# Performance work log

Measured on AMD Instinct MI355X. Metric: run time of the kernel, lower is better.

The kernel has to match this reference:

```python
import jax, jax.numpy as jnp
import numpy as np

B, S, H, E, V = 64, 512, 1024, 512, 32000
D = 2  # bidirectional encoder -> memory dim = D*H


def setup_inputs() -> dict:
    key = jax.random.key(0)
    ks = jax.random.split(key, 16)
    sc = lambda n: 1.0 / np.sqrt(n)
    return {
        "word": jax.random.randint(ks[0], (B,), 1, V),
        "hidden": jax.random.normal(ks[1], (B, H), jnp.float32),
        "encoder_outputs": jax.random.normal(ks[2], (B, S, D * H), jnp.float32),
        "output_distribution": jax.random.uniform(ks[3], (B, V), jnp.float32),
        "encoder_attention": jax.random.uniform(ks[4], (B, S), jnp.float32),
        # embedding (padding_idx=0 row zeroed)
        "emb": jax.random.normal(ks[5], (V, E), jnp.float32).at[0].set(0.0) * 0.02,
        # Bah_Attn params
        "lin1_w": jax.random.normal(ks[6], (H, H), jnp.float32) * sc(H),
        "lin1_b": jnp.zeros((H,), jnp.float32),
        "lin2_w": jax.random.normal(ks[7], (H, D * H), jnp.float32) * sc(D * H),
        "lin2_b": jnp.zeros((H,), jnp.float32),
        "v_w": jax.random.normal(ks[8], (1, H), jnp.float32) * sc(H),
        "v_b": jnp.zeros((1,), jnp.float32),
        # GRUCell params: input = context(2H) + word_vec(E) = 2560
        "W_ih": jax.random.normal(ks[9], (3 * H, D * H + E), jnp.float32) * sc(H),
        "b_ih": jnp.zeros((3 * H,), jnp.float32),
        "W_hh": jax.random.normal(ks[10], (3 * H, H), jnp.float32) * sc(H),
        "b_hh": jnp.zeros((3 * H,), jnp.float32),
        # output projection
        "out_w": jax.random.normal(ks[11], (V, H), jnp.float32) * sc(H),
        "out_b": jnp.zeros((V,), jnp.float32),
    }


def reference(word, hidden, encoder_outputs, output_distribution, encoder_attention,
              emb, lin1_w, lin1_b, lin2_w, lin2_b, v_w, v_b,
              W_ih, b_ih, W_hh, b_hh, out_w, out_b):
    # word embedding lookup (feed_word_emb='word')
    word_vec = emb[word]                                   # [B, E]
    h_x = hidden @ lin1_w.T + lin1_b                       # [B, H]
    h_m = jnp.einsum('bsm,hm->bsh', encoder_outputs, lin2_w) + lin2_b  # [B, S, H]
    e = jnp.tanh(h_x[:, None, :] + h_m) @ v_w[0] + v_b[0]  # [B, S]
    score = jax.nn.softmax(e, axis=-1)                     # [B, S]
    context = jnp.einsum('bs,bsm->bm', score, encoder_outputs)  # [B, 2H]
    # GRUCell step on cat([context, word_vec])
    x = jnp.concatenate([context, word_vec], axis=1)       # [B, 2H+E]
    gi = x @ W_ih.T + b_ih                                 # [B, 3H]
    gh = hidden @ W_hh.T + b_hh                            # [B, 3H]
    i_r, i_z, i_n = jnp.split(gi, 3, axis=1)
    h_r, h_z, h_n = jnp.split(gh, 3, axis=1)
    r = jax.nn.sigmoid(i_r + h_r)
    z = jax.nn.sigmoid(i_z + h_z)
    n = jnp.tanh(i_n + r * h_n)
    new_hidden = (1.0 - z) * n + z * hidden                # [B, H]
    pred_word = new_hidden @ out_w.T + out_b               # [B, V]
    return (pred_word, new_hidden, score)
```

## Files before the change

### kernel.cpp

```cpp
#include <hip/hip_runtime.h>
#include <hip/hip_bf16.h>
#include <stdint.h>

typedef __attribute__((ext_vector_type(4))) float f32x4;
typedef __attribute__((ext_vector_type(8))) short short8;

#define B_   64
#define S_   512
#define H_   1024
#define E_   512
#define V_   32000
#define M_   2048
#define BS_  32768
#define XIN_ 2560
#define G3_  3072

__device__ __forceinline__ unsigned short f2bf(float f) {
  union { float f; unsigned u; } x; x.f = f;
  unsigned r = x.u + 0x7fffu + ((x.u >> 16) & 1u);
  return (unsigned short)(r >> 16);
}

__device__ __forceinline__ float bf2f(unsigned short u) {
  union { unsigned u; float f; } x; x.u = (unsigned)u << 16; return x.f;
}

__device__ __forceinline__ void async16(const void* g, void* l) {
  __builtin_amdgcn_global_load_lds((const __attribute__((address_space(1))) unsigned*)g,
                                   (__attribute__((address_space(3))) unsigned*)l,
                                   16, 0, 0);
}

__global__ __launch_bounds__(256) void k_conv(const float* __restrict__ enc,
                                              unsigned short* __restrict__ ebf,
                                              const float* __restrict__ lin2w,
                                              unsigned short* __restrict__ bw,
                                              const int* __restrict__ word,
                                              const float* __restrict__ emb,
                                              float* __restrict__ wv) {
  const size_t NENC8 = (size_t)BS_ * M_ / 8;
  const size_t NW8   = (size_t)H_ * M_ / 8;
  const size_t NWV4  = (size_t)B_ * E_ / 4;
  const size_t total = NENC8 + NW8 + NWV4;
  for (size_t idx = (size_t)blockIdx.x * 256 + threadIdx.x; idx < total;
       idx += (size_t)gridDim.x * 256) {
    if (idx < NENC8) {
      f32x4 a = *(const f32x4*)(enc + idx * 8);
      f32x4 b = *(const f32x4*)(enc + idx * 8 + 4);
      short8 o = { (short)f2bf(a.x), (short)f2bf(a.y), (short)f2bf(a.z), (short)f2bf(a.w),
                   (short)f2bf(b.x), (short)f2bf(b.y), (short)f2bf(b.z), (short)f2bf(b.w) };
      *(short8*)(ebf + idx * 8) = o;
    } else if (idx < NENC8 + NW8) {
      size_t i = idx - NENC8;
      f32x4 a = *(const f32x4*)(lin2w + i * 8);
      f32x4 b = *(const f32x4*)(lin2w + i * 8 + 4);
      short8 o = { (short)f2bf(a.x), (short)f2bf(a.y), (short)f2bf(a.z), (short)f2bf(a.w),
                   (short)f2bf(b.x), (short)f2bf(b.y), (short)f2bf(b.z), (short)f2bf(b.w) };
      *(short8*)(bw + i * 8) = o;
    } else {
      size_t i = idx - NENC8 - NW8;
      int i0 = (int)i * 4;
      int b = i0 >> 9, c = i0 & 511;
      f32x4 v = *(const f32x4*)(emb + (size_t)word[b] * E_ + c);
      *(f32x4*)(wv + i0) = v;
    }
  }
}

__global__ __launch_bounds__(256) void k_hx(const float* __restrict__ hidden,
                                            const float* __restrict__ w1,
                                            const float* __restrict__ b1,
                                            const float* __restrict__ b2,
                                            float* __restrict__ hx) {
  __shared__ float hs[64][36];
  __shared__ float Ws[64][36];
  const int t = threadIdx.x;
  const int hbase = blockIdx.x * 64;
  const int hb = t & 15, bb = t >> 4;
  const int srow = t >> 2, sc0 = (t & 3) * 8;
  float acc[4][4] = {};
  for (int kc = 0; kc < H_; kc += 32) {
    *(f32x4*)&hs[srow][sc0]     = *(const f32x4*)(hidden + (size_t)srow * H_ + kc + sc0);
    *(f32x4*)&hs[srow][sc0 + 4] = *(const f32x4*)(hidden + (size_t)srow * H_ + kc + sc0 + 4);
    *(f32x4*)&Ws[srow][sc0]     = *(const f32x4*)(w1 + (size_t)(hbase + srow) * H_ + kc + sc0);
    *(f32x4*)&Ws[srow][sc0 + 4] = *(const f32x4*)(w1 + (size_t)(hbase + srow) * H_ + kc + sc0 + 4);
    __syncthreads();
#pragma unroll
    for (int kk = 0; kk < 32; ++kk) {
      float a[4], w4[4];
#pragma unroll
      for (int i = 0; i < 4; ++i) a[i] = hs[bb * 4 + i][kk];
#pragma unroll
      for (int j = 0; j < 4; ++j) w4[j] = Ws[hb + 16 * j][kk];
#pragma unroll
      for (int i = 0; i < 4; ++i)
#pragma unroll
        for (int j = 0; j < 4; ++j) acc[i][j] += a[i] * w4[j];
    }
    __syncthreads();
  }
#pragma unroll
  for (int i = 0; i < 4; ++i)
#pragma unroll
    for (int j = 0; j < 4; ++j) {
      int h = hbase + hb + 16 * j;
      hx[(size_t)(bb * 4 + i) * H_ + h] = acc[i][j] + b1[h] + b2[h];
    }
}

__global__ __launch_bounds__(256) void k_attn_bf(const unsigned short* __restrict__ encbf,
                                                 const unsigned short* __restrict__ bw,
                                                 const float* __restrict__ hx,
                                                 const float* __restrict__ vw,
                                                 float* __restrict__ epart) {
  __shared__ unsigned short As[3][4096];
  __shared__ unsigned short Bs[3][4096];
  const int bid = blockIdx.x;
  const int xcd = bid & 7, idx = bid >> 3;
  const int bm = xcd * 32 + (idx >> 3);
  const int bn = idx & 7;
  const int t = threadIdx.x;
  const int l = t & 63, w = t >> 6;
  const int wr = w >> 1, wc = w & 1;
  const int l15 = l & 15, l4 = l >> 4;

  f32x4 acc[4][4] = {};

  const unsigned short* Ag = encbf + (size_t)(bm * 128) * M_;
  const unsigned short* Bg = bw + (size_t)(bn * 128) * M_;

  const int srow = t >> 2;
  const int sc = ((t & 3) ^ ((t >> 3) & 3)) * 8;
  const unsigned short* ApT = Ag + (size_t)srow * M_ + sc;
  const unsigned short* BpT = Bg + (size_t)srow * M_ + sc;
  const int xoff = (l4 ^ ((l15 >> 1) & 3)) * 8;

#define STAGE(buf, kt) do { const int k0 = (kt) * 32;                    \
    async16(ApT + k0,             &As[buf][0]    + (size_t)t * 8);       \
    async16(ApT + 64 * M_ + k0,   &As[buf][2048] + (size_t)t * 8);       \
    async16(BpT + k0,             &Bs[buf][0]    + (size_t)t * 8);       \
    async16(BpT + 64 * M_ + k0,   &Bs[buf][2048] + (size_t)t * 8); } while (0)

  STAGE(0, 0);
  STAGE(1, 1);
  asm volatile("s_waitcnt vmcnt(4)" ::: "memory");
  __builtin_amdgcn_s_barrier();

  int cur = 0;
  for (int kt = 0; kt < 64; ++kt) {
    int nx2 = cur + 2; if (nx2 >= 3) nx2 -= 3;
    if (kt < 62) STAGE(nx2, kt + 2);
    short8 af[4], bf[4];
#pragma unroll
    for (int m = 0; m < 4; ++m)
      af[m] = *(const short8*)(&As[cur][(wr * 64 + m * 16 + l15) * 32 + xoff]);
#pragma unroll
    for (int n = 0; n < 4; ++n)
      bf[n] = *(const short8*)(&Bs[cur][(wc * 64 + n * 16 + l15) * 32 + xoff]);
#pragma unroll
    for (int m = 0; m < 4; ++m)
#pragma unroll
      for (int n = 0; n < 4; ++n)
        acc[m][n] = __builtin_amdgcn_mfma_f32_16x16x32_bf16(af[m], bf[n], acc[m][n], 0, 0, 0);
    if (kt < 62) {
      asm volatile("s_waitcnt vmcnt(4)" ::: "memory");
    } else {
      asm volatile("s_waitcnt vmcnt(0)" ::: "memory");
    }
    __builtin_amdgcn_s_barrier();
    cur = cur + 1; if (cur >= 3) cur = 0;
  }
#undef STAGE

  const int colbase = bn * 128 + wc * 64;
#pragma unroll
  for (int m = 0; m < 4; ++m) {
#pragma unroll
    for (int j = 0; j < 4; ++j) {
      int rloc = wr * 64 + m * 16 + l4 * 4 + j;
      int rg = bm * 128 + rloc;
      int b = rg >> 9;
      float sum = 0.f;
#pragma unroll
      for (int n = 0; n < 4; ++n) {
        int h = colbase + n * 16 + l15;
        sum += vw[h] * tanhf(hx[b * H_ + h] + acc[m][n][j]);
      }
      sum += __shfl_xor(sum, 1);
      sum += __shfl_xor(sum, 2);
      sum += __shfl_xor(sum, 4);
      sum += __shfl_xor(sum, 8);
      if (l15 == 0) epart[(size_t)(bn * 2 + wc) * BS_ + rg] = sum;
    }
  }
}

__global__ __launch_bounds__(256) void k_attn(const float* __restrict__ enc,
                                              const unsigned short* __restrict__ bw,
                                              const float* __restrict__ hx,
                                              const float* __restrict__ vw,
                                              float* __restrict__ epart) {
  __shared__ unsigned short As[128 * 32];
  __shared__ unsigned short Bs[128 * 32];
  const int bid = blockIdx.x;
  const int bm = bid & 255, bn = bid >> 8;
  const int t = threadIdx.x;
  const int l = t & 63, w = t >> 6;
  const int wr = w >> 1, wc = w & 1;
  const int l15 = l & 15, l4 = l >> 4;

  f32x4 acc[4][4] = {};

  const float* Ag = enc + (size_t)(bm * 128) * M_;
  const unsigned short* Bg = bw + (size_t)(bn * 128) * M_;

  const int ar = t >> 3;
  const int ac = (t & 7) * 4;
  const int br = t >> 2;
  const int bc = (t & 3) * 8;

  for (int kt = 0; kt < 64; ++kt) {
    const int k0 = kt * 32;
    async16(Bg + (size_t)br * M_ + k0 + bc, (char*)Bs + (size_t)t * 16);
    async16(Bg + (size_t)(br + 64) * M_ + k0 + bc, (char*)Bs + 4096 + (size_t)t * 16);
#pragma unroll
    for (int j = 0; j < 4; ++j) {
      f32x4 v = *(const f32x4*)(Ag + (size_t)(ar + j * 32) * M_ + k0 + ac);
      ushort4 o = { f2bf(v.x), f2bf(v.y), f2bf(v.z), f2bf(v.w) };
      *(ushort4*)(As + (ar + j * 32) * 32 + ac) = o;
    }
    __syncthreads();
    short8 af[4], bf[4];
#pragma unroll
    for (int m = 0; m < 4; ++m)
      af[m] = *(const short8*)(As + (wr * 64 + m * 16 + l15) * 32 + l4 * 8);
#pragma unroll
    for (int n = 0; n < 4; ++n)
      bf[n] = *(const short8*)(Bs + (wc * 64 + n * 16 + l15) * 32 + l4 * 8);
#pragma unroll
    for (int m = 0; m < 4; ++m)
#pragma unroll
      for (int n = 0; n < 4; ++n)
        acc[m][n] = __builtin_amdgcn_mfma_f32_16x16x32_bf16(af[m], bf[n], acc[m][n], 0, 0, 0);
    __syncthreads();
  }

  const int colbase = bn * 128 + wc * 64;
#pragma unroll
  for (int m = 0; m < 4; ++m) {
#pragma unroll
    for (int j = 0; j < 4; ++j) {
      int rloc = wr * 64 + m * 16 + l4 * 4 + j;
      int rg = bm * 128 + rloc;
      int b = rg >> 9;
      float sum = 0.f;
#pragma unroll
      for (int n = 0; n < 4; ++n) {
        int h = colbase + n * 16 + l15;
        sum += vw[h] * tanhf(hx[b * H_ + h] + acc[m][n][j]);
      }
      sum += __shfl_xor(sum, 1);
      sum += __shfl_xor(sum, 2);
      sum += __shfl_xor(sum, 4);
      sum += __shfl_xor(sum, 8);
      if (l15 == 0) epart[(size_t)(bn * 2 + wc) * BS_ + rg] = sum;
    }
  }
}

__global__ __launch_bounds__(256) void k_softmax(const float* __restrict__ epart,
                                                 float* __restrict__ score) {
  int b = blockIdx.x, t = threadIdx.x;
  float v0 = 0.f, v1 = 0.f;
#pragma unroll
  for (int p = 0; p < 16; ++p) {
    v0 += epart[(size_t)p * BS_ + b * S_ + t];
    v1 += epart[(size_t)p * BS_ + b * S_ + 256 + t];
  }
  int w = t >> 6, l = t & 63;
  float m = fmaxf(v0, v1);
#pragma unroll
  for (int off = 32; off; off >>= 1) m = fmaxf(m, __shfl_xor(m, off));
  __shared__ float sm[4];
  __shared__ float ssum[4];
  if (l == 0) sm[w] = m;
  __syncthreads();
  float M = fmaxf(fmaxf(sm[0], sm[1]), fmaxf(sm[2], sm[3]));
  float p0 = expf(v0 - M), p1 = expf(v1 - M);
  float s = p0 + p1;
#pragma unroll
  for (int off = 32; off; off >>= 1) s += __shfl_xor(s, off);
  if (l == 0) ssum[w] = s;
  __syncthreads();
  float inv = 1.f / (ssum[0] + ssum[1] + ssum[2] + ssum[3]);
  score[b * S_ + t] = p0 * inv;
  score[b * S_ + 256 + t] = p1 * inv;
}

__global__ __launch_bounds__(256) void k_ctxb(const unsigned short* __restrict__ encbf,
                                              const float* __restrict__ score,
                                              float* __restrict__ cpart) {
  int blk = blockIdx.x;
  int b = blk >> 3, sc = blk & 7;
  int t = threadIdx.x;
  int m = t * 8;
  f32x4 acc0 = {0.f, 0.f, 0.f, 0.f}, acc1 = {0.f, 0.f, 0.f, 0.f};
  const unsigned short* ep = encbf + (size_t)(b * S_ + sc * 64) * M_ + m;
  const float* sp = score + b * S_ + sc * 64;
#pragma unroll 4
  for (int s8 = 0; s8 < 64; ++s8) {
    float sv = sp[s8];
    short8 v = *(const short8*)(ep + (size_t)s8 * M_);
    acc0.x += bf2f((unsigned short)v[0]) * sv;
    acc0.y += bf2f((unsigned short)v[1]) * sv;
    acc0.z += bf2f((unsigned short)v[2]) * sv;
    acc0.w += bf2f((unsigned short)v[3]) * sv;
    acc1.x += bf2f((unsigned short)v[4]) * sv;
    acc1.y += bf2f((unsigned short)v[5]) * sv;
    acc1.z += bf2f((unsigned short)v[6]) * sv;
    acc1.w += bf2f((unsigned short)v[7]) * sv;
  }
  float* dst = cpart + (size_t)sc * (B_ * M_) + b * M_ + m;
  *(f32x4*)dst = acc0;
  *(f32x4*)(dst + 4) = acc1;
}

__global__ __launch_bounds__(256) void k_ctx(const float* __restrict__ enc,
                                             const float* __restrict__ score,
                                             float* __restrict__ cpart) {
  int blk = blockIdx.x;
  int b = blk >> 4, mc = (blk >> 3) & 1, sc = blk & 7;
  int t = threadIdx.x;
  int m = mc * 1024 + t * 4;
  f32x4 acc = {0.f, 0.f, 0.f, 0.f};
  const float* ep = enc + (size_t)b * S_ * M_ + m;
  const float* sp = score + b * S_ + sc * 64;
#pragma unroll 4
  for (int s8 = 0; s8 < 64; ++s8) {
    float sv = sp[s8];
    f32x4 v = *(const f32x4*)(ep + (size_t)(sc * 64 + s8) * M_);
    acc += v * sv;
  }
  *(f32x4*)(cpart + (size_t)sc * (B_ * M_) + b * M_ + m) = acc;
}

__global__ void k_ctxred(const float* __restrict__ cpart, float* __restrict__ ctx) {
  int i0 = (blockIdx.x * 256 + threadIdx.x) * 4;
  f32x4 a = {0.f, 0.f, 0.f, 0.f};
#pragma unroll
  for (int p = 0; p < 8; ++p) a += *(const f32x4*)(cpart + (size_t)p * (B_ * M_) + i0);
  *(f32x4*)(ctx + i0) = a;
}

__global__ __launch_bounds__(256) void k_grugemm(const float* __restrict__ ctx,
                                                 const float* __restrict__ wv,
                                                 const float* __restrict__ hidden,
                                                 const float* __restrict__ Wih,
                                                 const float* __restrict__ bih,
                                                 const float* __restrict__ Whh,
                                                 const float* __restrict__ bhh,
                                                 float* __restrict__ gi0,
                                                 float* __restrict__ gi1,
                                                 float* __restrict__ gh0,
                                                 float* __restrict__ gh1) {
  __shared__ float xs[64][36];
  __shared__ float Ws[64][36];
  const int t = threadIdx.x;
  const int blk = blockIdx.x;
  const bool ghh = blk >= 96;
  const int sub = ghh ? blk - 96 : blk;
  const int colt = sub % 48, half = sub / 48;
  const int gbase = colt * 64;
  const int K = ghh ? H_ : XIN_;
  const int klo = ghh ? (half ? 512 : 0) : (half ? 1280 : 0);
  const int khi = ghh ? (half ? 1024 : 512) : (half ? 2560 : 1280);
  const float* Wp = ghh ? Whh : Wih;
  const int vb = t & 15, bb = t >> 4;
  const int srow = t >> 2, sc0 = (t & 3) * 8;
  float acc[4][4] = {};
  for (int kc = klo; kc < khi; kc += 32) {
    f32x4 xa, xb;
    if (ghh) {
      xa = *(const f32x4*)(hidden + (size_t)srow * H_ + kc + sc0);
      xb = *(const f32x4*)(hidden + (size_t)srow * H_ + kc + sc0 + 4);
    } else if (kc + sc0 < M_) {
      xa = *(const f32x4*)(ctx + (size_t)srow * M_ + kc + sc0);
      xb = *(const f32x4*)(ctx + (size_t)srow * M_ + kc + sc0 + 4);
    } else {
      xa = *(const f32x4*)(wv + (size_t)srow * E_ + kc + sc0 - M_);
      xb = *(const f32x4*)(wv + (size_t)srow * E_ + kc + sc0 - M_ + 4);
    }
    *(f32x4*)&xs[srow][sc0] = xa;
    *(f32x4*)&xs[srow][sc0 + 4] = xb;
    *(f32x4*)&Ws[srow][sc0]     = *(const f32x4*)(Wp + (size_t)(gbase + srow) * K + kc + sc0);
    *(f32x4*)&Ws[srow][sc0 + 4] = *(const f32x4*)(Wp + (size_t)(gbase + srow) * K + kc + sc0 + 4);
    __syncthreads();
#pragma unroll
    for (int kk = 0; kk < 32; ++kk) {
      float a[4], w4[4];
#pragma unroll
      for (int i = 0; i < 4; ++i) a[i] = xs[bb * 4 + i][kk];
#pragma unroll
      for (int j = 0; j < 4; ++j) w4[j] = Ws[vb + 16 * j][kk];
#pragma unroll
      for (int i = 0; i < 4; ++i)
#pragma unroll
        for (int j = 0; j < 4; ++j) acc[i][j] += a[i] * w4[j];
    }
    __syncthreads();
  }
  float* dst = ghh ? (half ? gh1 : gh0) : (half ? gi1 : gi0);
  const float* bias = ghh ? bhh : bih;
#pragma unroll
  for (int i = 0; i < 4; ++i)
#pragma unroll
    for (int j = 0; j < 4; ++j) {
      int g = gbase + vb + 16 * j;
      float v = acc[i][j] + (half ? 0.f : bias[g]);
      dst[(size_t)(bb * 4 + i) * G3_ + g] = v;
    }
}

__global__ void k_gate(const float* __restrict__ gi0, const float* __restrict__ gi1,
                       const float* __restrict__ gh0, const float* __restrict__ gh1,
                       const float* __restrict__ hidden, float* __restrict__ newh,
                       unsigned short* __restrict__ newhbf) {
  int o = blockIdx.x * 256 + threadIdx.x;
  int b = o >> 10, h = o & 1023;
  size_t base = (size_t)b * G3_;
  float ir = gi0[base + h] + gi1[base + h];
  float iz = gi0[base + 1024 + h] + gi1[base + 1024 + h];
  float in = gi0[base + 2048 + h] + gi1[base + 2048 + h];
  float hr = gh0[base + h] + gh1[base + h];
  float hz = gh0[base + 1024 + h] + gh1[base + 1024 + h];
  float hn = gh0[base + 2048 + h] + gh1[base + 2048 + h];
  float r = 1.f / (1.f + expf(-(ir + hr)));
  float z = 1.f / (1.f + expf(-(iz + hz)));
  float n = tanhf(in + r * hn);
  float nh = (1.f - z) * n + z * hidden[o];
  newh[o] = nh;
  newhbf[o] = f2bf(nh);
}

__global__ __launch_bounds__(256) void k_outproj_mfma(const unsigned short* __restrict__ newhbf,
                                                      const float* __restrict__ ow,
                                                      const float* __restrict__ ob,
                                                      float* __restrict__ pred) {
  __shared__ unsigned short As[2048];
  __shared__ unsigned short Bs[4096];
  const int t = threadIdx.x;
  const int w = t >> 6, l = t & 63;
  const int l15 = l & 15, l4 = l >> 4;
  const int vbase = blockIdx.x * 128;

  const unsigned short* aSrc = newhbf + (size_t)(t & 63) * H_ + (t >> 6) * 8;
  const int br = t >> 1, bh = t & 1;
  const float* bSrc = ow + (size_t)(vbase + br) * H_ + bh * 16;

  f32x4 acc[4][2] = {};

  for (int kc = 0; kc < H_; kc += 32) {
    async16(aSrc + kc, (char*)As + (size_t)t * 16);
    f32x4 v0 = *(const f32x4*)(bSrc + kc);
    f32x4 v1 = *(const f32x4*)(bSrc + kc + 4);
    f32x4 v2 = *(const f32x4*)(bSrc + kc + 8);
    f32x4 v3 = *(const f32x4*)(bSrc + kc + 12);
    ushort4 p0 = { f2bf(v0.x), f2bf(v0.y), f2bf(v0.z), f2bf(v0.w) };
    ushort4 p1 = { f2bf(v1.x), f2bf(v1.y), f2bf(v1.z), f2bf(v1.w) };
    ushort4 p2 = { f2bf(v2.x), f2bf(v2.y), f2bf(v2.z), f2bf(v2.w) };
    ushort4 p3 = { f2bf(v3.x), f2bf(v3.y), f2bf(v3.z), f2bf(v3.w) };
    const int kg0 = bh * 2;
    *(ushort4*)(Bs + kg0 * 1024 + br * 8)       = p0;
    *(ushort4*)(Bs + kg0 * 1024 + br * 8 + 4)   = p1;
    *(ushort4*)(Bs + (kg0 + 1) * 1024 + br * 8)     = p2;
    *(ushort4*)(Bs + (kg0 + 1) * 1024 + br * 8 + 4) = p3;
    __syncthreads();
    short8 af[4], bf[2];
#pragma unroll
    for (int rf = 0; rf < 4; ++rf)
      af[rf] = *(const short8*)(As + l4 * 512 + (rf * 16 + l15) * 8);
#pragma unroll
    for (int cf = 0; cf < 2; ++cf)
      bf[cf] = *(const short8*)(Bs + l4 * 1024 + (w * 32 + cf * 16 + l15) * 8);
#pragma unroll
    for (int rf = 0; rf < 4; ++rf)
#pragma unroll
      for (int cf = 0; cf < 2; ++cf)
        acc[rf][cf] = __builtin_amdgcn_mfma_f32_16x16x32_bf16(af[rf], bf[cf], acc[rf][cf], 0, 0, 0);
    __syncthreads();
  }

#pragma unroll
  for (int cf = 0; cf < 2; ++cf) {
    int col = vbase + w * 32 + cf * 16 + l15;
    float bias = ob[col];
#pragma unroll
    for (int rf = 0; rf < 4; ++rf)
#pragma unroll
      for (int j = 0; j < 4; ++j) {
        int row = rf * 16 + l4 * 4 + j;
        pred[(size_t)row * V_ + col] = acc[rf][cf][j] + bias;
      }
  }
}

extern "C" void kernel_launch(void* const* d_in, const int* in_sizes, int n_in,
                              void* d_out, int out_size, void* d_ws, size_t ws_size,
                              hipStream_t stream) {
  const int*   word   = (const int*)d_in[0];
  const float* hidden = (const float*)d_in[1];
  const float* enc    = (const float*)d_in[2];
  const float* emb    = (const float*)d_in[5];
  const float* lin1w  = (const float*)d_in[6];
  const float* lin1b  = (const float*)d_in[7];
  const float* lin2w  = (const float*)d_in[8];
  const float* lin2b  = (const float*)d_in[9];
  const float* vw     = (const float*)d_in[10];
  const float* Wih    = (const float*)d_in[12];
  const float* bih    = (const float*)d_in[13];
  const float* Whh    = (const float*)d_in[14];
  const float* bhh    = (const float*)d_in[15];
  const float* ow     = (const float*)d_in[16];
  const float* ob     = (const float*)d_in[17];

  float* out   = (float*)d_out;
  float* pred  = out;
  float* newh  = out + 2048000;
  float* score = out + 2113536;

  const size_t ENCBF = 134217728;
  const bool fast = ws_size >= ENCBF + 13107200;
  char* ws = (char*)d_ws;
  unsigned short* encbf = (unsigned short*)ws;
  size_t base = fast ? ENCBF : 0;
  unsigned short* bw = (unsigned short*)(ws + base);
  float* hx    = (float*)(ws + base + 4194304);
  float* wvbuf = (float*)(ws + base + 4456448);
  float* epart = (float*)(ws + base + 4587520);
  float* cpart = (float*)(ws + base + 6684672);
  float* ctx   = (float*)(ws + base + 10878976);
  float* gi0   = (float*)(ws + base + 11403264);
  float* gh0   = (float*)(ws + base + 12189696);
  unsigned short* nhbf = (unsigned short*)(ws + base + 12976128);
  float* gi1   = epart;
  float* gh1   = epart + 196608;

  k_hx<<<16, 256, 0, stream>>>(hidden, lin1w, lin1b, lin2b, hx);
  if (fast) {
    k_conv<<<4096, 256, 0, stream>>>(enc, encbf, lin2w, bw, word, emb, wvbuf);
    k_attn_bf<<<2048, 256, 0, stream>>>(encbf, bw, hx, vw, epart);
    k_softmax<<<64, 256, 0, stream>>>(epart, score);
    k_ctxb<<<512, 256, 0, stream>>>(encbf, score, cpart);
  } else {
    k_conv<<<4096, 256, 0, stream>>>(enc, encbf, lin2w, bw, word, emb, wvbuf);
    k_attn<<<2048, 256, 0, stream>>>(enc, bw, hx, vw, epart);
    k_softmax<<<64, 256, 0, stream>>>(epart, score);
    k_ctx<<<1024, 256, 0, stream>>>(enc, score, cpart);
  }
  k_ctxred<<<128, 256, 0, stream>>>(cpart, ctx);
  k_grugemm<<<192, 256, 0, stream>>>(ctx, wvbuf, hidden, Wih, bih, Whh, bhh, gi0, gi1, gh0, gh1);
  k_gate<<<256, 256, 0, stream>>>(gi0, gi1, gh0, gh1, hidden, newh, nhbf);
  k_outproj_mfma<<<250, 256, 0, stream>>>(nhbf, ow, ob, pred);
}
```

Before: 503.4 us.

## Add 256x128-tile 8-wave bf16 MFMA attention GEMM with triple-buffered async loads

Adds a new attention-score kernel that computes 256x128 output tiles per 512-thread block instead of the previous smaller tiles, using triple-buffered async global-to-LDS copies with XOR-swizzled layout and priority hints around the MFMA loop. The fused tanh/v-weight reduction epilogue is kept. Larger tiles raise operand reuse and halve the block count, aiming to cut LDS/global traffic in the dominant encoder GEMM. It needs 72 KB of dynamic shared memory set via a function attribute, falls back to the old kernel if that fails, and risks lower occupancy.

```diff
diff --git a/kernel.cpp b/kernel.cpp
--- a/kernel.cpp
+++ b/kernel.cpp
@@ -106,6 +106,98 @@
       int h = hbase + hb + 16 * j;
       hx[(size_t)(bb * 4 + i) * H_ + h] = acc[i][j] + b1[h] + b2[h];
     }
+}
+
+__global__ __launch_bounds__(512, 4) void k_attn2(const unsigned short* __restrict__ encbf,
+                                                  const unsigned short* __restrict__ bw,
+                                                  const float* __restrict__ hx,
+                                                  const float* __restrict__ vw,
+                                                  float* __restrict__ epart) {
+  extern __shared__ char smem[];
+  const int t = threadIdx.x;
+  const int w8 = t >> 6, l = t & 63;
+  const int wm = w8 >> 1, wn = w8 & 1;
+  const int l15 = l & 15, l4 = l >> 4;
+  const int bid = blockIdx.x;
+  const int xcd = bid & 7, idx = bid >> 3;
+  const int bm = xcd * 16 + (idx >> 3);
+  const int bn = idx & 7;
+  const int b = bm >> 1;
+
+  f32x4 acc[4][4] = {};
+
+  const unsigned short* Ag = encbf + (size_t)(bm * 256) * M_;
+  const unsigned short* Bg = bw + (size_t)(bn * 128) * M_;
+
+  const int lr = l >> 2, lc = l & 3;
+  const int sw = (lr >> 1) & 3;
+  const unsigned short* aSrc0 = Ag + (size_t)(w8 * 32 + lr) * M_ + (lc ^ sw) * 8;
+  const unsigned short* aSrc1 = aSrc0 + (size_t)16 * M_;
+  const unsigned short* bSrc  = Bg + (size_t)(w8 * 16 + lr) * M_ + (lc ^ sw) * 8;
+  const int slotoff = (l4 ^ ((l15 >> 1) & 3)) * 16;
+
+#define STAGE(buf, kt) do { const int k0 = (kt) * 32;                       \
+    char* base_ = smem + (buf) * 24576;                                     \
+    async16(aSrc0 + k0, base_ + w8 * 2048 + l * 16);                        \
+    async16(aSrc1 + k0, base_ + w8 * 2048 + 1024 + l * 16);                 \
+    async16(bSrc  + k0, base_ + 16384 + w8 * 1024 + l * 16); } while (0)
+
+  STAGE(0, 0);
+  STAGE(1, 1);
+  asm volatile("s_waitcnt vmcnt(3)" ::: "memory");
+  __builtin_amdgcn_s_barrier();
+
+  int cur = 0;
+  for (int kt = 0; kt < 64; ++kt) {
+    int nx2 = cur + 2; if (nx2 >= 3) nx2 -= 3;
+    if (kt < 62) STAGE(nx2, kt + 2);
+    const char* aBase = smem + cur * 24576;
+    const char* bBase = aBase + 16384;
+    short8 af[4], bf[4];
+#pragma unroll
+    for (int m = 0; m < 4; ++m)
+      af[m] = *(const short8*)(aBase + (wm * 64 + m * 16 + l15) * 64 + slotoff);
+#pragma unroll
+    for (int n = 0; n < 4; ++n)
+      bf[n] = *(const short8*)(bBase + (wn * 64 + n * 16 + l15) * 64 + slotoff);
+    __builtin_amdgcn_s_setprio(1);
+#pragma unroll
+    for (int m = 0; m < 4; ++m)
+#pragma unroll
+      for (int n = 0; n < 4; ++n)
+        acc[m][n] = __builtin_amdgcn_mfma_f32_16x16x32_bf16(af[m], bf[n], acc[m][n], 0, 0, 0);
+    __builtin_amdgcn_s_setprio(0);
+    if (kt < 62) {
+      asm volatile("s_waitcnt vmcnt(3)" ::: "memory");
+    } else {
+      asm volatile("s_waitcnt vmcnt(0)" ::: "memory");
+    }
+    __builtin_amdgcn_s_barrier();
+    cur = cur + 1; if (cur >= 3) cur = 0;
+  }
+#undef STAGE
+
+  const int rbase = bm * 256 + wm * 64;
+  const int colbase = bn * 128 + wn * 64;
+  const int part = bn * 2 + wn;
+#pragma unroll
+  for (int m = 0; m < 4; ++m) {
+#pragma unroll
+    for (int j = 0; j < 4; ++j) {
+      int rg = rbase + m * 16 + l4 * 4 + j;
+      float sum = 0.f;
+#pragma unroll
+      for (int n = 0; n < 4; ++n) {
+        int h = colbase + n * 16 + l15;
+        sum += vw[h] * tanhf(hx[b * H_ + h] + acc[m][n][j]);
+      }
+      sum += __shfl_xor(sum, 1);
+      sum += __shfl_xor(sum, 2);
+      sum += __shfl_xor(sum, 4);
+      sum += __shfl_xor(sum, 8);
+      if (l15 == 0) epart[(size_t)part * BS_ + rg] = sum;
+    }
+  }
 }
 
 __global__ __launch_bounds__(256) void k_attn_bf(const unsigned short* __restrict__ encbf,
@@ -545,10 +637,21 @@
   float* gi1   = epart;
   float* gh1   = epart + 196608;
 
+  bool use2 = false;
+  if (fast) {
+    hipError_t e = hipFuncSetAttribute((const void*)k_attn2,
+        hipFuncAttributeMaxDynamicSharedMemorySize, 73728);
+    use2 = (e == hipSuccess);
+  }
+
   k_hx<<<16, 256, 0, stream>>>(hidden, lin1w, lin1b, lin2b, hx);
   if (fast) {
     k_conv<<<4096, 256, 0, stream>>>(enc, encbf, lin2w, bw, word, emb, wvbuf);
-    k_attn_bf<<<2048, 256, 0, stream>>>(encbf, bw, hx, vw, epart);
+    if (use2) {
+      k_attn2<<<1024, 512, 73728, stream>>>(encbf, bw, hx, vw, epart);
+    } else {
+      k_attn_bf<<<2048, 256, 0, stream>>>(encbf, bw, hx, vw, epart);
+    }
     k_softmax<<<64, 256, 0, stream>>>(epart, score);
     k_ctxb<<<512, 256, 0, stream>>>(encbf, score, cpart);
   } else {
```

Result: faster. 463.1 us (-8.0%).
